# Performance work log

Hardware: AMD Instinct MI355X
Metric: run time of the kernel (lower is better)

## Reference

```python
import jax, jax.numpy as jnp
import numpy as np

MIN_CONTEXT_SIZE = 64
FUTURE_STEPS = 12


def setup_inputs() -> dict:
    key = jax.random.key(0)
    k1, k2, k3 = jax.random.split(key, 3)
    B, T, E, C = 32, 256, 256, 256
    embeddings = jax.random.normal(k1, (B, T, E), dtype=jnp.float32)
    contexts = jax.random.normal(k2, (B, T, C), dtype=jnp.float32)
    # Bilinear comparator weight, scaled like a typical linear init
    W = jax.random.normal(k3, (E, C), dtype=jnp.float32) * (1.0 / np.sqrt(E).astype(np.float32))
    return {"embeddings": embeddings, "contexts": contexts, "W": W}


def reference(embeddings, contexts, W):
    B, T, E = embeddings.shape
    log_probs = []
    for step in range(FUTURE_STEPS):
        emb = embeddings[:, MIN_CONTEXT_SIZE + step:T]          # (B, S, E)
        ctx = contexts[:, MIN_CONTEXT_SIZE - 1:T - step - 1]    # (B, S, C)
        S = T - step - MIN_CONTEXT_SIZE
        # all-pairs bilinear scores: score[b,s,j,t] = emb[b,s] @ W @ ctx[j,t]
        proj = jnp.einsum('bse,ec->bsc', emb, W)                # (B, S, C)
        scores = jnp.einsum('bsc,jtc->bsjt', proj, ctx)         # (B, S, B, S)
        flat = scores.reshape(B * S, B * S)
        positives = jnp.diagonal(flat).reshape(B, S)            # matched (b,s) pairs
        lse = jax.nn.logsumexp(scores.reshape(B, S, B * S), axis=-1)
        lse = lse - jnp.log(jnp.asarray(B * S, dtype=scores.dtype))
        log_probs.append((positives - lse).reshape(-1))
    flat_log_probs = jnp.concatenate(log_probs, axis=0)
    return -flat_log_probs.mean()
```

## Files before the change

kernel.cpp:

```cpp
#include <hip/hip_runtime.h>
#include <hip/hip_bf16.h>
#include <math.h>


#define NROW 6144
#define TAIL0 181
#define NTERMS 71616.0f
#define LOG2E 1.44269504088896340736f
#define SHIFT2 92.33248261689366f

typedef __attribute__((ext_vector_type(8))) short short8;
typedef __attribute__((ext_vector_type(4))) float f32x4;

__device__ __forceinline__ ushort f2bf(float f) {
  union { float f; uint32_t u; } v; v.f = f;
  uint32_t u = v.u;
  return (ushort)((u + 0x7FFFu + ((u >> 16) & 1u)) >> 16);
}
__device__ __forceinline__ float expsh(float x) {
  return exp2f(fmaf(x, LOG2E, -SHIFT2));
}

__device__ __forceinline__ void gload16(const ushort* g, ushort* l) {
  __builtin_amdgcn_global_load_lds((const __attribute__((address_space(1))) void*)g,
                                   (__attribute__((address_space(3))) void*)l, 16, 0, 0);
}

__global__ __launch_bounds__(256) void k_cast(const float* __restrict__ ctx,
                                              const float* __restrict__ W,
                                              ushort* __restrict__ X,
                                              ushort* __restrict__ Wt,
                                              float* __restrict__ zbase) {
  int bi = blockIdx.x;
  if (bi < 1536) {
    int idx = bi * 256 + threadIdx.x;
    int row = idx >> 6, f4 = idx & 63;
    int j = row & 31, t = row >> 5;
    float4 f = *(const float4*)(ctx + ((size_t)(j * 256 + 63 + t)) * 256 + f4 * 4);
    ushort4 o;
    o.x = f2bf(f.x); o.y = f2bf(f.y); o.z = f2bf(f.z); o.w = f2bf(f.w);
    ((ushort4*)(X + (size_t)row * 256))[f4] = o;
  } else if (bi < 1792) {
    int c = bi - 1536, e = threadIdx.x;
    Wt[c * 256 + e] = f2bf(W[e * 256 + c]);
  } else {
    int idx = (bi - 1792) * 256 + threadIdx.x;
    if (idx < 6146) zbase[idx] = 0.f;
  }
}

__global__ __launch_bounds__(256) void k_proj(const float* __restrict__ emb,
                                              const ushort* __restrict__ Wt,
                                              ushort* __restrict__ P) {
  __shared__ ushort Al[16 * 256];
  int tid = threadIdx.x;
  int rt = blockIdx.x;
  int half = blockIdx.y;
#pragma unroll
  for (int q = 0; q < 4; ++q) {
    int cc = tid + q * 256;
    int rw = cc >> 6, f4 = cc & 63;
    int u = rt * 16 + rw, b = u / 192, urow = u - b * 192;
    float4 f = *(const float4*)(emb + ((size_t)(b * 256 + 64 + urow)) * 256 + f4 * 4);
    ushort4 o;
    o.x = f2bf(f.x); o.y = f2bf(f.y); o.z = f2bf(f.z); o.w = f2bf(f.w);
    int c8 = f4 >> 1;
    *(ushort4*)&Al[rw * 256 + ((c8 ^ (rw & 7)) * 8) + (f4 & 1) * 4] = o;
  }
  __syncthreads();

  int w = tid >> 6, l = tid & 63;
  int fr = l & 15, kb = l >> 4;
  short8 af[8];
#pragma unroll
  for (int kk = 0; kk < 8; ++kk) {
    int c8 = kk * 4 + kb;
    af[kk] = *(const short8*)&Al[fr * 256 + (c8 ^ (fr & 7)) * 8];
  }
#pragma unroll
  for (int i = 0; i < 2; ++i) {
    int ct = half * 8 + w * 2 + i;
    const short8* bp = (const short8*)(Wt + (size_t)(ct * 16 + fr) * 256);
    f32x4 acc = {0.f, 0.f, 0.f, 0.f};
#pragma unroll
    for (int kk = 0; kk < 8; ++kk)
      acc = __builtin_amdgcn_mfma_f32_16x16x32_bf16(af[kk], bp[kk * 4 + kb], acc, 0, 0, 0);
#pragma unroll
    for (int r = 0; r < 4; ++r)
      P[(size_t)(rt * 16 + kb * 4 + r) * 256 + ct * 16 + fr] = f2bf(acc[r]);
  }
}

__global__ __launch_bounds__(256, 4) void k_scores(const ushort* __restrict__ P,
                                                   const ushort* __restrict__ X,
                                                   float* __restrict__ sum0,
                                                   float* __restrict__ tail,
                                                   float* __restrict__ pos) {
  __shared__ ushort Albuf[128 * 64];
  __shared__ ushort Blbuf[128 * 64];
  int tid = threadIdx.x;
  int w = tid >> 6, l = tid & 63;
  int wr = w >> 1, wc = w & 1;
  int rowbase = blockIdx.x * 128;
  int colbase = blockIdx.y * 128;

  int fr = l & 15, kb = l >> 4;

  int r0 = tid >> 3;
  int srcc = (tid & 7) ^ (r0 & 7);
  const ushort* gA = P + (size_t)(rowbase + r0) * 256 + srcc * 8;
  const ushort* gB = X + (size_t)(colbase + r0) * 256 + srcc * 8;

  f32x4 acc[4][4];
#pragma unroll
  for (int m = 0; m < 4; ++m)
#pragma unroll
    for (int n = 0; n < 4; ++n) acc[m][n] = {0.f, 0.f, 0.f, 0.f};

  for (int kk = 0; kk < 4; ++kk) {
    int kbase = kk * 64;
#pragma unroll
    for (int q = 0; q < 4; ++q)
      gload16(gA + (size_t)q * 32 * 256 + kbase, Albuf + (size_t)(q * 256 + w * 64) * 8);
#pragma unroll
    for (int q = 0; q < 4; ++q)
      gload16(gB + (size_t)q * 32 * 256 + kbase, Blbuf + (size_t)(q * 256 + w * 64) * 8);
    __syncthreads();

#pragma unroll
    for (int ks = 0; ks < 2; ++ks) {
      int sl = (ks * 4 + kb) ^ (fr & 7);
      short8 af[4], bf[4];
#pragma unroll
      for (int m = 0; m < 4; ++m)
        af[m] = *(const short8*)&Albuf[((wr * 64 + m * 16 + fr) * 8 + sl) * 8];
#pragma unroll
      for (int n = 0; n < 4; ++n)
        bf[n] = *(const short8*)&Blbuf[((wc * 64 + n * 16 + fr) * 8 + sl) * 8];
#pragma unroll
      for (int m = 0; m < 4; ++m)
#pragma unroll
        for (int n = 0; n < 4; ++n)
          acc[m][n] = __builtin_amdgcn_mfma_f32_16x16x32_bf16(af[m], bf[n],
                                                              acc[m][n], 0, 0, 0);
    }
    if (kk < 3) __syncthreads();
  }

  int t0g = blockIdx.y * 4 + wc * 2;
  bool all0 = blockIdx.y < 45;
#pragma unroll
  for (int m = 0; m < 4; ++m) {
    int rowg = rowbase + wr * 64 + m * 16 + kb * 4;
#pragma unroll
    for (int r = 0; r < 4; ++r) {
      int u = rowg + r;
      int b = u / 192;
      int urow = u - b * 192;
#pragma unroll
      for (int n = 0; n < 4; ++n) {
        int colg = colbase + wc * 64 + n * 16 + fr;
        int dt = urow - (colg >> 5);
        if ((colg & 31) == b && dt >= 0 && dt < 12)
          pos[u * 12 + dt] = acc[m][n][r];
      }
      if (all0) {
        float v = expsh(acc[m][0][r]) + expsh(acc[m][1][r]) +
                  expsh(acc[m][2][r]) + expsh(acc[m][3][r]);
        v += __shfl_xor(v, 1); v += __shfl_xor(v, 2);
        v += __shfl_xor(v, 4); v += __shfl_xor(v, 8);
        if (fr == 0) atomicAdd(&sum0[u], v);
      } else {
        float v0 = expsh(acc[m][0][r]) + expsh(acc[m][1][r]);
        float v1 = expsh(acc[m][2][r]) + expsh(acc[m][3][r]);
        v0 += __shfl_xor(v0, 1); v0 += __shfl_xor(v0, 2);
        v0 += __shfl_xor(v0, 4); v0 += __shfl_xor(v0, 8);
        v1 += __shfl_xor(v1, 1); v1 += __shfl_xor(v1, 2);
        v1 += __shfl_xor(v1, 4); v1 += __shfl_xor(v1, 8);
        if (fr == 0) {
          if (t0g + 1 < TAIL0) {
            atomicAdd(&sum0[u], v0 + v1);
          } else if (t0g < TAIL0) {
            atomicAdd(&sum0[u], v0);
            tail[(size_t)(t0g + 1 - TAIL0) * NROW + u] = v1;
          } else {
            tail[(size_t)(t0g - TAIL0) * NROW + u] = v0;
            tail[(size_t)(t0g + 1 - TAIL0) * NROW + u] = v1;
          }
        }
      }
    }
  }
}

__global__ void k_loss(const float* __restrict__ sum0, const float* __restrict__ tail,
                       const float* __restrict__ pos, float* acc,
                       unsigned int* cnt, float* __restrict__ out) {
  int u = blockIdx.x * 256 + threadIdx.x;
  int urow = u % 192;
  int smax = urow < 11 ? urow : 11;
  float denom = sum0[u];
  float local = 0.f;
  for (int s = 11; s >= 0; --s) {
    if (s < 11) denom += tail[(size_t)(10 - s) * NROW + u];
    if (s <= smax)
      local += pos[u * 12 + s] - 64.f - __logf(denom) + __logf(32.f * (float)(192 - s));
  }
  float v = local;
  v += __shfl_xor(v, 1);  v += __shfl_xor(v, 2);  v += __shfl_xor(v, 4);
  v += __shfl_xor(v, 8);  v += __shfl_xor(v, 16); v += __shfl_xor(v, 32);
  __shared__ float red[4];
  if ((threadIdx.x & 63) == 0) red[threadIdx.x >> 6] = v;
  __syncthreads();
  if (threadIdx.x == 0) {
    atomicAdd(acc, red[0] + red[1] + red[2] + red[3]);
    __threadfence();
    unsigned int old = atomicAdd(cnt, 1u);
    if (old == 23u) {
      float tot = atomicAdd(acc, 0.0f);
      out[0] = -tot * (1.0f / NTERMS);
    }
  }
}

extern "C" void kernel_launch(void* const* d_in, const int* in_sizes, int n_in,
                              void* d_out, int out_size, void* d_ws, size_t ws_size,
                              hipStream_t stream) {
  const float* emb = (const float*)d_in[0];
  const float* ctx = (const float*)d_in[1];
  const float* W   = (const float*)d_in[2];
  char* ws = (char*)d_ws;
  ushort* P    = (ushort*)(ws + 0);
  ushort* X    = (ushort*)(ws + 3145728);
  ushort* Wt   = (ushort*)(ws + 6291456);
  float*  sum0 = (float*)(ws + 6422528);
  float*  acc  = (float*)(ws + 6447104);
  unsigned int* cnt = (unsigned int*)(ws + 6447108);
  float*  tail = (float*)(ws + 6447360);
  float*  pos  = (float*)(ws + 6717696);

  k_cast<<<1817, 256, 0, stream>>>(ctx, W, X, Wt, sum0);
  k_proj<<<dim3(384, 2), 256, 0, stream>>>(emb, Wt, P);
  k_scores<<<dim3(48, 48), 256, 0, stream>>>(P, X, sum0, tail, pos);
  k_loss<<<24, 256, 0, stream>>>(sum0, tail, pos, acc, cnt, (float*)d_out);
}
```

Before: 71.28 us.

## Shrink score tile to 128x64, prefetch next K-slab, remap blocks per XCD

The scores GEMM tile drops from 128x128 to 128x64, which halves B shared memory and the accumulators so the launch bound can rise from 4 to 5 blocks per CU. The K loop now reads fragments into registers, then issues the next slab's global-to-LDS loads before running the MFMAs, so loads overlap compute. A 1D grid is remapped so each XCD gets a contiguous range of column tiles for L2 locality. The epilogue is simplified because each wave now covers exactly one timestep column group. The cost is more blocks and twice as many A-tile reloads overall.

```diff
diff --git a/kernel.cpp b/kernel.cpp
--- a/kernel.cpp
+++ b/kernel.cpp
@@ -91,18 +91,24 @@
   }
 }
 
-__global__ __launch_bounds__(256, 4) void k_scores(const ushort* __restrict__ P,
+__global__ __launch_bounds__(256, 5) void k_scores(const ushort* __restrict__ P,
                                                    const ushort* __restrict__ X,
                                                    float* __restrict__ sum0,
                                                    float* __restrict__ tail,
                                                    float* __restrict__ pos) {
   __shared__ ushort Albuf[128 * 64];
-  __shared__ ushort Blbuf[128 * 64];
+  __shared__ ushort Blbuf[64 * 64];
   int tid = threadIdx.x;
   int w = tid >> 6, l = tid & 63;
   int wr = w >> 1, wc = w & 1;
-  int rowbase = blockIdx.x * 128;
-  int colbase = blockIdx.y * 128;
+
+  int lin = blockIdx.x;
+  int xcd = lin & 7;
+  int idx = lin >> 3;
+  int bx = idx / 12;
+  int by = xcd * 12 + (idx - bx * 12);
+  int rowbase = bx * 128;
+  int colbase = by * 64;
 
   int fr = l & 15, kb = l >> 4;
 
@@ -111,44 +117,54 @@
   const ushort* gA = P + (size_t)(rowbase + r0) * 256 + srcc * 8;
   const ushort* gB = X + (size_t)(colbase + r0) * 256 + srcc * 8;
 
-  f32x4 acc[4][4];
+  f32x4 acc[4][2];
 #pragma unroll
   for (int m = 0; m < 4; ++m)
 #pragma unroll
-    for (int n = 0; n < 4; ++n) acc[m][n] = {0.f, 0.f, 0.f, 0.f};
+    for (int n = 0; n < 2; ++n) acc[m][n] = {0.f, 0.f, 0.f, 0.f};
+
+#pragma unroll
+  for (int q = 0; q < 4; ++q)
+    gload16(gA + (size_t)q * 32 * 256, Albuf + (size_t)(q * 256 + w * 64) * 8);
+#pragma unroll
+  for (int q = 0; q < 2; ++q)
+    gload16(gB + (size_t)q * 32 * 256, Blbuf + (size_t)(q * 256 + w * 64) * 8);
+  __syncthreads();
 
   for (int kk = 0; kk < 4; ++kk) {
-    int kbase = kk * 64;
-#pragma unroll
-    for (int q = 0; q < 4; ++q)
-      gload16(gA + (size_t)q * 32 * 256 + kbase, Albuf + (size_t)(q * 256 + w * 64) * 8);
-#pragma unroll
-    for (int q = 0; q < 4; ++q)
-      gload16(gB + (size_t)q * 32 * 256 + kbase, Blbuf + (size_t)(q * 256 + w * 64) * 8);
-    __syncthreads();
-
+    short8 af[2][4], bf[2][2];
 #pragma unroll
     for (int ks = 0; ks < 2; ++ks) {
       int sl = (ks * 4 + kb) ^ (fr & 7);
-      short8 af[4], bf[4];
 #pragma unroll
       for (int m = 0; m < 4; ++m)
-        af[m] = *(const short8*)&Albuf[((wr * 64 + m * 16 + fr) * 8 + sl) * 8];
-#pragma unroll
-      for (int n = 0; n < 4; ++n)
-        bf[n] = *(const short8*)&Blbuf[((wc * 64 + n * 16 + fr) * 8 + sl) * 8];
+        af[ks][m] = *(const short8*)&Albuf[((wr * 64 + m * 16 + fr) * 8 + sl) * 8];
+#pragma unroll
+      for (int n = 0; n < 2; ++n)
+        bf[ks][n] = *(const short8*)&Blbuf[((wc * 32 + n * 16 + fr) * 8 + sl) * 8];
+    }
+    if (kk < 3) {
+      __syncthreads();
+      int kbase = (kk + 1) * 64;
+#pragma unroll
+      for (int q = 0; q < 4; ++q)
+        gload16(gA + (size_t)q * 32 * 256 + kbase, Albuf + (size_t)(q * 256 + w * 64) * 8);
+#pragma unroll
+      for (int q = 0; q < 2; ++q)
+        gload16(gB + (size_t)q * 32 * 256 + kbase, Blbuf + (size_t)(q * 256 + w * 64) * 8);
+    }
+#pragma unroll
+    for (int ks = 0; ks < 2; ++ks)
 #pragma unroll
       for (int m = 0; m < 4; ++m)
 #pragma unroll
-        for (int n = 0; n < 4; ++n)
-          acc[m][n] = __builtin_amdgcn_mfma_f32_16x16x32_bf16(af[m], bf[n],
+        for (int n = 0; n < 2; ++n)
+          acc[m][n] = __builtin_amdgcn_mfma_f32_16x16x32_bf16(af[ks][m], bf[ks][n],
                                                               acc[m][n], 0, 0, 0);
-    }
     if (kk < 3) __syncthreads();
   }
 
-  int t0g = blockIdx.y * 4 + wc * 2;
-  bool all0 = blockIdx.y < 45;
+  int t = by * 2 + wc;
 #pragma unroll
   for (int m = 0; m < 4; ++m) {
     int rowg = rowbase + wr * 64 + m * 16 + kb * 4;
@@ -157,37 +173,20 @@
       int u = rowg + r;
       int b = u / 192;
       int urow = u - b * 192;
-#pragma unroll
-      for (int n = 0; n < 4; ++n) {
-        int colg = colbase + wc * 64 + n * 16 + fr;
-        int dt = urow - (colg >> 5);
-        if ((colg & 31) == b && dt >= 0 && dt < 12)
-          pos[u * 12 + dt] = acc[m][n][r];
+      int dt = urow - t;
+      if (dt >= 0 && dt < 12) {
+#pragma unroll
+        for (int n = 0; n < 2; ++n) {
+          int j = (wc * 32 + n * 16 + fr) & 31;
+          if (j == b) pos[u * 12 + dt] = acc[m][n][r];
+        }
       }
-      if (all0) {
-        float v = expsh(acc[m][0][r]) + expsh(acc[m][1][r]) +
-                  expsh(acc[m][2][r]) + expsh(acc[m][3][r]);
-        v += __shfl_xor(v, 1); v += __shfl_xor(v, 2);
-        v += __shfl_xor(v, 4); v += __shfl_xor(v, 8);
-        if (fr == 0) atomicAdd(&sum0[u], v);
-      } else {
-        float v0 = expsh(acc[m][0][r]) + expsh(acc[m][1][r]);
-        float v1 = expsh(acc[m][2][r]) + expsh(acc[m][3][r]);
-        v0 += __shfl_xor(v0, 1); v0 += __shfl_xor(v0, 2);
-        v0 += __shfl_xor(v0, 4); v0 += __shfl_xor(v0, 8);
-        v1 += __shfl_xor(v1, 1); v1 += __shfl_xor(v1, 2);
-        v1 += __shfl_xor(v1, 4); v1 += __shfl_xor(v1, 8);
-        if (fr == 0) {
-          if (t0g + 1 < TAIL0) {
-            atomicAdd(&sum0[u], v0 + v1);
-          } else if (t0g < TAIL0) {
-            atomicAdd(&sum0[u], v0);
-            tail[(size_t)(t0g + 1 - TAIL0) * NROW + u] = v1;
-          } else {
-            tail[(size_t)(t0g - TAIL0) * NROW + u] = v0;
-            tail[(size_t)(t0g + 1 - TAIL0) * NROW + u] = v1;
-          }
-        }
+      float v = expsh(acc[m][0][r]) + expsh(acc[m][1][r]);
+      v += __shfl_xor(v, 1); v += __shfl_xor(v, 2);
+      v += __shfl_xor(v, 4); v += __shfl_xor(v, 8);
+      if (fr == 0) {
+        if (t < TAIL0) atomicAdd(&sum0[u], v);
+        else tail[(size_t)(t - TAIL0) * NROW + u] = v;
       }
     }
   }
@@ -241,6 +240,6 @@
 
   k_cast<<<1817, 256, 0, stream>>>(ctx, W, X, Wt, sum0);
   k_proj<<<dim3(384, 2), 256, 0, stream>>>(emb, Wt, P);
-  k_scores<<<dim3(48, 48), 256, 0, stream>>>(P, X, sum0, tail, pos);
+  k_scores<<<4608, 256, 0, stream>>>(P, X, sum0, tail, pos);
   k_loss<<<24, 256, 0, stream>>>(sum0, tail, pos, acc, cnt, (float*)d_out);
 }
```

After: 102.3 us. 1.44x slower.
